# Performance work log

Hardware: AMD Instinct MI355X
Metric: run time of the kernel (lower is better)

## Reference

```python
import jax, jax.numpy as jnp
import numpy as np

SEQ, BATCH, NFEAT, HID = 512, 128, 64, 256


def setup_inputs() -> dict:
    key = jax.random.key(0)
    ks = jax.random.split(key, 11)
    s = 0.05
    return {
        "X": jax.random.normal(ks[0], (SEQ, BATCH, NFEAT), jnp.float32),
        "w_ih0": jax.random.normal(ks[1], (4 * HID, NFEAT), jnp.float32) * s,
        "w_hh0": jax.random.normal(ks[2], (4 * HID, HID), jnp.float32) * s,
        "b_ih0": jax.random.normal(ks[3], (4 * HID,), jnp.float32) * s,
        "b_hh0": jax.random.normal(ks[4], (4 * HID,), jnp.float32) * s,
        "w_ih1": jax.random.normal(ks[5], (4 * HID, HID), jnp.float32) * s,
        "w_hh1": jax.random.normal(ks[6], (4 * HID, HID), jnp.float32) * s,
        "b_ih1": jax.random.normal(ks[7], (4 * HID,), jnp.float32) * s,
        "b_hh1": jax.random.normal(ks[8], (4 * HID,), jnp.float32) * s,
        "fc_w": jax.random.normal(ks[9], (1, HID), jnp.float32) * s,
        "fc_b": jax.random.normal(ks[10], (1,), jnp.float32) * s,
    }


def _lstm_layer(x, w_ih, w_hh, b_ih, b_hh):
    # x: [S, B, F]; PyTorch gate order: i, f, g, o along the 4H axis.
    S, B, _ = x.shape
    H = w_hh.shape[1]
    # Precompute input projection for all timesteps (batched GEMM).
    xp = jnp.einsum("sbf,gf->sbg", x, w_ih) + b_ih + b_hh  # [S, B, 4H]
    w_hh_t = w_hh.T  # [H, 4H]

    def step(carry, xt):
        h, c = carry
        gates = xt + h @ w_hh_t  # [B, 4H]
        i, f, g, o = jnp.split(gates, 4, axis=-1)
        i = jax.nn.sigmoid(i)
        f = jax.nn.sigmoid(f)
        g = jnp.tanh(g)
        o = jax.nn.sigmoid(o)
        c = f * c + i * g
        h = o * jnp.tanh(c)
        return (h, c), h

    h0 = jnp.zeros((B, H), x.dtype)
    c0 = jnp.zeros((B, H), x.dtype)
    _, out = jax.lax.scan(step, (h0, c0), xp)
    return out  # [S, B, H]


def reference(X, w_ih0, w_hh0, b_ih0, b_hh0, w_ih1, w_hh1, b_ih1, b_hh1, fc_w, fc_b):
    out0 = _lstm_layer(X, w_ih0, w_hh0, b_ih0, b_hh0)
    out1 = _lstm_layer(out0, w_ih1, w_hh1, b_ih1, b_hh1)
    last = out1[-1]  # [B, H]
    return last @ fc_w.T + fc_b  # [B, 1]
```

## Files before the change

kernel.cpp:

```cpp
#include <hip/hip_runtime.h>

#define SEQ   512
#define BATCH 128
#define NFEAT 64
#define HID   256
#define HB    (BATCH * HID)
#define NGRP  8
#define GBLK  32


typedef unsigned u32;
typedef unsigned long long u64;
typedef __attribute__((ext_vector_type(8))) short  short8;
typedef __attribute__((ext_vector_type(4))) float  f32x4;
typedef __attribute__((ext_vector_type(4))) unsigned short us4;

__device__ __forceinline__ unsigned short f2bf(float f) {
    union { float f; unsigned u; } c; c.f = f;
    unsigned r = c.u + 0x7FFF + ((c.u >> 16) & 1);
    return (unsigned short)(r >> 16);
}
__device__ __forceinline__ float bf2f(unsigned short h) {
    union { float f; unsigned u; } c; c.u = ((unsigned)h) << 16;
    return c.f;
}

__device__ __forceinline__ u64 ald64(const u64* p) {
    return __hip_atomic_load(p, __ATOMIC_RELAXED, __HIP_MEMORY_SCOPE_AGENT);
}
__device__ __forceinline__ u32 ald32(const u32* p) {
    return __hip_atomic_load(p, __ATOMIC_RELAXED, __HIP_MEMORY_SCOPE_AGENT);
}
__device__ __forceinline__ void ast32(u32* p, u32 v) {
    __hip_atomic_store(p, v, __ATOMIC_RELAXED, __HIP_MEMORY_SCOPE_AGENT);
}

__global__ __launch_bounds__(256, 1) void lstm_persist(
    const float* __restrict__ X,
    const float* __restrict__ w_ih0,
    const float* __restrict__ w_hh0,
    const float* __restrict__ b_ih0,
    const float* __restrict__ b_hh0,
    const float* __restrict__ w_ih1,
    const float* __restrict__ w_hh1,
    const float* __restrict__ b_ih1,
    const float* __restrict__ b_hh1,
    u32* __restrict__ h0p,
    u32* __restrict__ h1p,
    u32* __restrict__ flags)
{
    const int bid = blockIdx.x;
    const int tid = threadIdx.x;
    const int g     = bid >> 5;
    const int rk    = bid & 31;
    const int layer = rk >> 4;
    const int ct    = rk & 15;
    const int b0    = g * 16;
    const int j0    = ct * 16;

    const int wave = tid >> 6;
    const int l    = tid & 63;
    const int kq   = l >> 4;
    const int ar   = l & 15;

    __shared__ __align__(16) unsigned short hsh[16 * 512];
    __shared__ __align__(16) unsigned short hsl[16 * 512];
    __shared__ float red[4][4][16][20];
    __shared__ float bbuf[4][16];

    {
        const short8 z8 = {0, 0, 0, 0, 0, 0, 0, 0};
        for (int i = tid; i < 16 * 512 / 8; i += 256) {
            ((short8*)hsh)[i] = z8;
            ((short8*)hsl)[i] = z8;
        }
    }
    if (tid < 64) {
        const int gg = tid >> 4, cc = tid & 15;
        const float* bi_ = layer ? b_ih1 : b_ih0;
        const float* bh_ = layer ? b_hh1 : b_hh0;
        bbuf[gg][cc] = bi_[gg * 256 + j0 + cc] + bh_[gg * 256 + j0 + cc];
    }

    short8 Ahi[4][4], Alo[4][4];
    {
        const short8 z8 = {0, 0, 0, 0, 0, 0, 0, 0};
        #pragma unroll
        for (int gg = 0; gg < 4; ++gg) {
            const int row = gg * 256 + j0 + ar;
            #pragma unroll
            for (int kt = 0; kt < 4; ++kt) {
                const int k = (wave * 4 + kt) * 32 + kq * 8;
                const float* src = nullptr;
                if (layer) {
                    src = (k < 256) ? (w_ih1 + (size_t)row * 256 + k)
                                    : (w_hh1 + (size_t)row * 256 + (k - 256));
                } else {
                    if (k < 64)       src = w_ih0 + (size_t)row * 64 + k;
                    else if (k < 320) src = w_hh0 + (size_t)row * 256 + (k - 64);
                }
                short8 hi8 = z8, lo8 = z8;
                if (src) {
                    const float4 a = ((const float4*)src)[0];
                    const float4 b = ((const float4*)src)[1];
                    const float wv[8] = {a.x, a.y, a.z, a.w, b.x, b.y, b.z, b.w};
                    #pragma unroll
                    for (int i = 0; i < 8; ++i) {
                        const unsigned short h = f2bf(wv[i]);
                        hi8[i] = (short)h;
                        lo8[i] = (short)f2bf(wv[i] - bf2f(h));
                    }
                }
                Ahi[gg][kt] = hi8;
                Alo[gg][kt] = lo8;
            }
        }
    }

    const int eb = tid >> 4, ecc = tid & 15;
    float creg = 0.f;

    u32* hown  = layer ? h1p : h0p;
    u32* gflag = flags + (size_t)g * GBLK * 32;
    const int hoff = layer ? 256 : 64;

    const int pb = tid >> 4, pf = tid & 15;
    float4 xpf = make_float4(0.f, 0.f, 0.f, 0.f);
    if (!layer)
        xpf = ((const float4*)(X + (size_t)(b0 + pb) * NFEAT))[pf];

    __syncthreads();

    for (int t = 0; t < SEQ; ++t) {
        {
            u32 thr;
            int idx;
            if (tid < 16) {
                idx = layer * 16 + tid;
                thr = (u32)t;
                if (tid == ct) thr = 0;
            } else {
                idx = (1 - layer) * 16 + (tid - 16);
                thr = layer ? (u32)(t + 1) : (u32)(t > 0 ? t - 1 : 0);
            }
            if (tid < 32 && thr > 0) {
                int guard = 0;
                while (ald32(&gflag[idx * 32]) < thr && ++guard < (1 << 18)) {}
            }
            __syncthreads();
        }

        const int par = t & 1, pp = par ^ 1;
        const int b = tid >> 4, f0 = tid & 15;
        const int swz = (b & 7) << 3;

        if (t > 0) {
            const u64* hp = (const u64*)(hown + (size_t)pp * HB
                                         + (size_t)(b0 + b) * HID + f0 * 16);
            u64 v[8];
            #pragma unroll
            for (int i = 0; i < 8; ++i) v[i] = ald64(hp + i);
            short8 h0v, l0v, h1v, l1v;
            #pragma unroll
            for (int i = 0; i < 4; ++i) {
                const u32 w0 = (u32)v[i], w1 = (u32)(v[i] >> 32);
                h0v[2*i]   = (short)(w0 >> 16); l0v[2*i]   = (short)(w0 & 0xffff);
                h0v[2*i+1] = (short)(w1 >> 16); l0v[2*i+1] = (short)(w1 & 0xffff);
                const u32 w2 = (u32)v[i+4], w3 = (u32)(v[i+4] >> 32);
                h1v[2*i]   = (short)(w2 >> 16); l1v[2*i]   = (short)(w2 & 0xffff);
                h1v[2*i+1] = (short)(w3 >> 16); l1v[2*i+1] = (short)(w3 & 0xffff);
            }
            const int us = b * 512 + hoff + f0 * 16;
            *(short8*)&hsh[us ^ swz]       = h0v;
            *(short8*)&hsh[(us + 8) ^ swz] = h1v;
            *(short8*)&hsl[us ^ swz]       = l0v;
            *(short8*)&hsl[(us + 8) ^ swz] = l1v;
        }
        if (layer) {
            const u64* xp = (const u64*)(h0p + (size_t)par * HB
                                         + (size_t)(b0 + b) * HID + f0 * 16);
            u64 v[8];
            #pragma unroll
            for (int i = 0; i < 8; ++i) v[i] = ald64(xp + i);
            short8 h0v, l0v, h1v, l1v;
            #pragma unroll
            for (int i = 0; i < 4; ++i) {
                const u32 w0 = (u32)v[i], w1 = (u32)(v[i] >> 32);
                h0v[2*i]   = (short)(w0 >> 16); l0v[2*i]   = (short)(w0 & 0xffff);
                h0v[2*i+1] = (short)(w1 >> 16); l0v[2*i+1] = (short)(w1 & 0xffff);
                const u32 w2 = (u32)v[i+4], w3 = (u32)(v[i+4] >> 32);
                h1v[2*i]   = (short)(w2 >> 16); l1v[2*i]   = (short)(w2 & 0xffff);
                h1v[2*i+1] = (short)(w3 >> 16); l1v[2*i+1] = (short)(w3 & 0xffff);
            }
            const int us = b * 512 + f0 * 16;
            *(short8*)&hsh[us ^ swz]       = h0v;
            *(short8*)&hsh[(us + 8) ^ swz] = h1v;
            *(short8*)&hsl[us ^ swz]       = l0v;
            *(short8*)&hsl[(us + 8) ^ swz] = l1v;
        } else {
            const float xv[4] = {xpf.x, xpf.y, xpf.z, xpf.w};
            us4 xh, xl;
            #pragma unroll
            for (int i = 0; i < 4; ++i) {
                const unsigned short hh = f2bf(xv[i]);
                xh[i] = hh;
                xl[i] = f2bf(xv[i] - bf2f(hh));
            }
            const int us = pb * 512 + pf * 4;
            const int sw = (pb & 7) << 3;
            *(us4*)&hsh[us ^ sw] = xh;
            *(us4*)&hsl[us ^ sw] = xl;
        }
        __syncthreads();

        if (!layer && t + 1 < SEQ)
            xpf = ((const float4*)(X + (size_t)(t + 1) * BATCH * NFEAT
                                     + (size_t)(b0 + pb) * NFEAT))[pf];

        {
            f32x4 acc[4];
            #pragma unroll
            for (int gg = 0; gg < 4; ++gg)
                acc[gg] = (f32x4){0.f, 0.f, 0.f, 0.f};

            #pragma unroll
            for (int kt = 0; kt < 4; ++kt) {
                const int KT = wave * 4 + kt;
                const int us = ar * 512 + KT * 32 + kq * 8;
                const int uswz = us ^ ((ar & 7) << 3);
                const short8 bh = *(const short8*)&hsh[uswz];
                const short8 bl = *(const short8*)&hsl[uswz];
                #pragma unroll
                for (int gg = 0; gg < 4; ++gg)
                    acc[gg] = __builtin_amdgcn_mfma_f32_16x16x32_bf16(
                        Ahi[gg][kt], bh, acc[gg], 0, 0, 0);
                #pragma unroll
                for (int gg = 0; gg < 4; ++gg)
                    acc[gg] = __builtin_amdgcn_mfma_f32_16x16x32_bf16(
                        Alo[gg][kt], bh, acc[gg], 0, 0, 0);
                #pragma unroll
                for (int gg = 0; gg < 4; ++gg)
                    acc[gg] = __builtin_amdgcn_mfma_f32_16x16x32_bf16(
                        Ahi[gg][kt], bl, acc[gg], 0, 0, 0);
            }
            #pragma unroll
            for (int gg = 0; gg < 4; ++gg)
                *(f32x4*)&red[wave][gg][ar][kq * 4] = acc[gg];
        }
        __syncthreads();

        {
            float p[4];
            #pragma unroll
            for (int gg = 0; gg < 4; ++gg)
                p[gg] = bbuf[gg][ecc] + red[0][gg][eb][ecc] + red[1][gg][eb][ecc]
                                      + red[2][gg][eb][ecc] + red[3][gg][eb][ecc];
            const float ig  = 1.0f / (1.0f + __expf(-p[0]));
            const float fg  = 1.0f / (1.0f + __expf(-p[1]));
            const float gg_ = tanhf(p[2]);
            const float og  = 1.0f / (1.0f + __expf(-p[3]));
            creg = fg * creg + ig * gg_;
            const float hv = og * tanhf(creg);
            const unsigned short hi = f2bf(hv);
            const unsigned short lo = f2bf(hv - bf2f(hi));
            ast32(&hown[(size_t)par * HB + (size_t)(b0 + eb) * HID + j0 + ecc],
                  ((u32)hi << 16) | (u32)lo);
        }

        __syncthreads();
        if (tid == 0)
            ast32(&gflag[rk * 32], (u32)(t + 1));
    }
}

__global__ __launch_bounds__(64) void fc_kernel(
    const u32* __restrict__ h1last_p,
    const float* __restrict__ fc_w,
    const float* __restrict__ fc_b,
    float* __restrict__ out)
{
    const int b    = blockIdx.x;
    const int lane = threadIdx.x;
    float sum = 0.0f;
    #pragma unroll
    for (int k = lane; k < HID; k += 64) {
        const u32 w = h1last_p[(size_t)b * HID + k];
        const float h = bf2f((unsigned short)(w >> 16))
                      + bf2f((unsigned short)(w & 0xffff));
        sum += h * fc_w[k];
    }
    #pragma unroll
    for (int off = 32; off > 0; off >>= 1)
        sum += __shfl_down(sum, off);
    if (lane == 0) out[b] = sum + fc_b[0];
}

extern "C" void kernel_launch(void* const* d_in, const int* in_sizes, int n_in,
                              void* d_out, int out_size, void* d_ws, size_t ws_size,
                              hipStream_t stream)
{
    const float* X     = (const float*)d_in[0];
    const float* w_ih0 = (const float*)d_in[1];
    const float* w_hh0 = (const float*)d_in[2];
    const float* b_ih0 = (const float*)d_in[3];
    const float* b_hh0 = (const float*)d_in[4];
    const float* w_ih1 = (const float*)d_in[5];
    const float* w_hh1 = (const float*)d_in[6];
    const float* b_ih1 = (const float*)d_in[7];
    const float* b_hh1 = (const float*)d_in[8];
    const float* fc_w  = (const float*)d_in[9];
    const float* fc_b  = (const float*)d_in[10];

    u32* h0p   = (u32*)d_ws;
    u32* h1p   = h0p + 2 * HB;
    u32* flags = h1p + 2 * HB;

    const size_t zbytes = (size_t)(4 * HB + NGRP * GBLK * 32) * sizeof(u32);
    (void)hipMemsetAsync(d_ws, 0, zbytes, stream);

    lstm_persist<<<NGRP * GBLK, 256, 0, stream>>>(X,
        w_ih0, w_hh0, b_ih0, b_hh0,
        w_ih1, w_hh1, b_ih1, b_hh1,
        h0p, h1p, flags);

    fc_kernel<<<BATCH, 64, 0, stream>>>(h1p + HB, fc_w, fc_b, (float*)d_out);
}
```

Measured before the change: 2.102 ms.

## Embed step tags in hidden-state words and use 4-deep ring buffers

Replaces the per-step flag spin-wait before reading h with polling the hidden-state words themselves, which now carry a 2-bit step tag in the low bits of the bf16 residual. Buffers grow from double to quadruple, so producers only need loose flag-based back-pressure a few steps behind. The end-of-step barrier is removed and the flag store moves earlier. This aims to cut per-step synchronisation latency on the serial recurrence, at the cost of two bits of low-part precision and more polling traffic on global memory.

```diff
diff --git a/kernel.cpp b/kernel.cpp
--- a/kernel.cpp
+++ b/kernel.cpp
@@ -33,6 +33,14 @@
 }
 __device__ __forceinline__ void ast32(u32* p, u32 v) {
     __hip_atomic_store(p, v, __ATOMIC_RELAXED, __HIP_MEMORY_SCOPE_AGENT);
+}
+__device__ __forceinline__ void agld16(const u32* p, u32 w[16]) {
+    const u64* q = (const u64*)p;
+    #pragma unroll
+    for (int i = 0; i < 8; ++i) {
+        const u64 v = ald64(q + i);
+        w[2 * i] = (u32)v; w[2 * i + 1] = (u32)(v >> 32);
+    }
 }
 
 __global__ __launch_bounds__(256, 1) void lstm_persist(
@@ -132,43 +140,43 @@
     __syncthreads();
 
     for (int t = 0; t < SEQ; ++t) {
-        {
-            u32 thr;
-            int idx;
-            if (tid < 16) {
-                idx = layer * 16 + tid;
-                thr = (u32)t;
-                if (tid == ct) thr = 0;
-            } else {
-                idx = (1 - layer) * 16 + (tid - 16);
-                thr = layer ? (u32)(t + 1) : (u32)(t > 0 ? t - 1 : 0);
-            }
-            if (tid < 32 && thr > 0) {
-                int guard = 0;
-                while (ald32(&gflag[idx * 32]) < thr && ++guard < (1 << 18)) {}
-            }
-            __syncthreads();
-        }
-
-        const int par = t & 1, pp = par ^ 1;
+        const int sp  = (t - 1) & 3;
+        const int st  = t & 3;
+        const u32 tgp = (t > 0) ? ((u32)((t - 1) >> 2) % 3u) + 1u : 0u;
+        const u32 tgc = ((u32)(t >> 2) % 3u) + 1u;
+
+        const u32* faddr = nullptr;
+        u32 fthr = 0, fval = 0;
+        if (tid < 16) {
+            if (tid != ct && t >= 3) {
+                faddr = &gflag[(layer * 16 + tid) * 32];
+                fthr  = (u32)(t - 2);
+            }
+        } else if (tid < 32 && layer == 0 && t >= 4) {
+            faddr = &gflag[(16 + (tid - 16)) * 32];
+            fthr  = (u32)(t - 3);
+        }
+        if (faddr) fval = ald32(faddr);
+
         const int b = tid >> 4, f0 = tid & 15;
         const int swz = (b & 7) << 3;
 
         if (t > 0) {
-            const u64* hp = (const u64*)(hown + (size_t)pp * HB
-                                         + (size_t)(b0 + b) * HID + f0 * 16);
-            u64 v[8];
-            #pragma unroll
-            for (int i = 0; i < 8; ++i) v[i] = ald64(hp + i);
+            const u32* hp = hown + (size_t)sp * HB + (size_t)(b0 + b) * HID + f0 * 16;
+            u32 w[16];
+            int guard = 0;
+            for (;;) {
+                agld16(hp, w);
+                bool ok = true;
+                #pragma unroll
+                for (int i = 0; i < 16; ++i) ok &= ((w[i] & 3u) == tgp);
+                if (ok || ++guard >= (1 << 14)) break;
+            }
             short8 h0v, l0v, h1v, l1v;
             #pragma unroll
-            for (int i = 0; i < 4; ++i) {
-                const u32 w0 = (u32)v[i], w1 = (u32)(v[i] >> 32);
-                h0v[2*i]   = (short)(w0 >> 16); l0v[2*i]   = (short)(w0 & 0xffff);
-                h0v[2*i+1] = (short)(w1 >> 16); l0v[2*i+1] = (short)(w1 & 0xffff);
-                const u32 w2 = (u32)v[i+4], w3 = (u32)(v[i+4] >> 32);
-                h1v[2*i]   = (short)(w2 >> 16); l1v[2*i]   = (short)(w2 & 0xffff);
-                h1v[2*i+1] = (short)(w3 >> 16); l1v[2*i+1] = (short)(w3 & 0xffff);
+            for (int i = 0; i < 8; ++i) {
+                h0v[i] = (short)(w[i] >> 16);     l0v[i] = (short)(w[i] & 0xFFFCu);
+                h1v[i] = (short)(w[8 + i] >> 16); l1v[i] = (short)(w[8 + i] & 0xFFFCu);
             }
             const int us = b * 512 + hoff + f0 * 16;
             *(short8*)&hsh[us ^ swz]       = h0v;
@@ -177,20 +185,21 @@
             *(short8*)&hsl[(us + 8) ^ swz] = l1v;
         }
         if (layer) {
-            const u64* xp = (const u64*)(h0p + (size_t)par * HB
-                                         + (size_t)(b0 + b) * HID + f0 * 16);
-            u64 v[8];
-            #pragma unroll
-            for (int i = 0; i < 8; ++i) v[i] = ald64(xp + i);
+            const u32* xp = h0p + (size_t)st * HB + (size_t)(b0 + b) * HID + f0 * 16;
+            u32 w[16];
+            int guard = 0;
+            for (;;) {
+                agld16(xp, w);
+                bool ok = true;
+                #pragma unroll
+                for (int i = 0; i < 16; ++i) ok &= ((w[i] & 3u) == tgc);
+                if (ok || ++guard >= (1 << 14)) break;
+            }
             short8 h0v, l0v, h1v, l1v;
             #pragma unroll
-            for (int i = 0; i < 4; ++i) {
-                const u32 w0 = (u32)v[i], w1 = (u32)(v[i] >> 32);
-                h0v[2*i]   = (short)(w0 >> 16); l0v[2*i]   = (short)(w0 & 0xffff);
-                h0v[2*i+1] = (short)(w1 >> 16); l0v[2*i+1] = (short)(w1 & 0xffff);
-                const u32 w2 = (u32)v[i+4], w3 = (u32)(v[i+4] >> 32);
-                h1v[2*i]   = (short)(w2 >> 16); l1v[2*i]   = (short)(w2 & 0xffff);
-                h1v[2*i+1] = (short)(w3 >> 16); l1v[2*i+1] = (short)(w3 & 0xffff);
+            for (int i = 0; i < 8; ++i) {
+                h0v[i] = (short)(w[i] >> 16);     l0v[i] = (short)(w[i] & 0xFFFCu);
+                h1v[i] = (short)(w[8 + i] >> 16); l1v[i] = (short)(w[8 + i] & 0xFFFCu);
             }
             const int us = b * 512 + f0 * 16;
             *(short8*)&hsh[us ^ swz]       = h0v;
@@ -204,14 +213,22 @@
             for (int i = 0; i < 4; ++i) {
                 const unsigned short hh = f2bf(xv[i]);
                 xh[i] = hh;
-                xl[i] = f2bf(xv[i] - bf2f(hh));
+                xl[i] = (unsigned short)(f2bf(xv[i] - bf2f(hh)) & 0xFFFF);
             }
             const int us = pb * 512 + pf * 4;
             const int sw = (pb & 7) << 3;
             *(us4*)&hsh[us ^ sw] = xh;
             *(us4*)&hsl[us ^ sw] = xl;
         }
+
+        if (faddr) {
+            int guard = 0;
+            while (fval < fthr && ++guard < (1 << 16)) fval = ald32(faddr);
+        }
         __syncthreads();
+
+        if (tid == 0)
+            ast32(&gflag[rk * 32], (u32)(t + 1));
 
         if (!layer && t + 1 < SEQ)
             xpf = ((const float4*)(X + (size_t)(t + 1) * BATCH * NFEAT
@@ -263,13 +280,9 @@
             const float hv = og * tanhf(creg);
             const unsigned short hi = f2bf(hv);
             const unsigned short lo = f2bf(hv - bf2f(hi));
-            ast32(&hown[(size_t)par * HB + (size_t)(b0 + eb) * HID + j0 + ecc],
-                  ((u32)hi << 16) | (u32)lo);
-        }
-
-        __syncthreads();
-        if (tid == 0)
-            ast32(&gflag[rk * 32], (u32)(t + 1));
+            ast32(&hown[(size_t)st * HB + (size_t)(b0 + eb) * HID + j0 + ecc],
+                  ((u32)hi << 16) | ((u32)lo & 0xFFFCu) | tgc);
+        }
     }
 }
 
@@ -286,7 +299,7 @@
     for (int k = lane; k < HID; k += 64) {
         const u32 w = h1last_p[(size_t)b * HID + k];
         const float h = bf2f((unsigned short)(w >> 16))
-                      + bf2f((unsigned short)(w & 0xffff));
+                      + bf2f((unsigned short)(w & 0xFFFCu));
         sum += h * fc_w[k];
     }
     #pragma unroll
@@ -312,10 +325,10 @@
     const float* fc_b  = (const float*)d_in[10];
 
     u32* h0p   = (u32*)d_ws;
-    u32* h1p   = h0p + 2 * HB;
-    u32* flags = h1p + 2 * HB;
-
-    const size_t zbytes = (size_t)(4 * HB + NGRP * GBLK * 32) * sizeof(u32);
+    u32* h1p   = h0p + 4 * HB;
+    u32* flags = h1p + 4 * HB;
+
+    const size_t zbytes = (size_t)(8 * HB + NGRP * GBLK * 32) * sizeof(u32);
     (void)hipMemsetAsync(d_ws, 0, zbytes, stream);
 
     lstm_persist<<<NGRP * GBLK, 256, 0, stream>>>(X,
@@ -323,5 +336,5 @@
         w_ih1, w_hh1, b_ih1, b_hh1,
         h0p, h1p, flags);
 
-    fc_kernel<<<BATCH, 64, 0, stream>>>(h1p + HB, fc_w, fc_b, (float*)d_out);
-}
+    fc_kernel<<<BATCH, 64, 0, stream>>>(h1p + 3 * HB, fc_w, fc_b, (float*)d_out);
+}
```

Result: slower. 2.199 ms (+4.6%).
